# Optimization experiments

Hardware: AMD Instinct MI355X
Metric: run time of the kernel (lower is better)

The kernel has to match this reference:

```python
import jax, jax.numpy as jnp
import numpy as np

GAMMA = 3.0
R = 0.02
ALPHA_RAISE = 1.0
DW_FLOOR = 0.0
B, D, G = 2097152, 16, 2048


def _annuity_factor(tau):
    # |R| >= 1e-12, so closed form branch of _annuity_factor
    return (1.0 - jnp.exp(-R * tau)) / R


def setup_inputs() -> dict:
    key = jax.random.key(0)
    k1, k2, k3, k4, k5 = jax.random.split(key, 5)
    X = jax.random.uniform(k1, (B, 2), jnp.float32, 0.1, 2.0)      # [wealth, habit] > 0
    TmT = jax.random.uniform(k2, (B, 1), jnp.float32, 0.0, 1.0)    # time-to-maturity tau
    y = jax.random.uniform(k3, (B, 1), jnp.float32, 0.1, 1.0)      # shadow price (lambda)
    u_star = jax.random.uniform(k4, (D,), jnp.float32, 0.0, 1.0)   # Merton weights buffer
    s_grid = jnp.linspace(0.0, 1.0, G).astype(jnp.float32)         # sorted tau grid
    z_tilde = jax.random.uniform(k5, (G,), jnp.float32, 0.5, 1.5)  # RIM boundary values
    return {"X": X, "TmT": TmT, "y": y, "u_star": u_star, "s_grid": s_grid, "z_tilde": z_tilde}


def reference(X, TmT, y, u_star, s_grid, z_tilde):
    wealth = X[:, :1]
    habit = X[:, 1:2]
    tau = TmT

    # z*(t) = linear interpolation of z_tilde over s_grid (replaces CPU bisect loop)
    s = jnp.clip(tau.reshape(-1), 0.0, s_grid[-1])
    z_tau = jnp.interp(s, s_grid, z_tilde).reshape(tau.shape)

    # hit-and-raise: CRRA boundary consumption C_boundary = (z/y)^{1/gamma}
    y_eff = jnp.clip(y, 1e-12, None)
    c_on_boundary = jnp.power(jnp.clip(z_tau / y_eff, 1e-24, None), 1.0 / GAMMA)
    need_raise = (y_eff * jnp.power(habit, GAMMA)) <= z_tau
    c_raised = ALPHA_RAISE * c_on_boundary + (1.0 - ALPHA_RAISE) * habit
    C = jnp.where(need_raise, jnp.maximum(c_raised, habit), habit)
    # c_softcap is None -> no cap

    pvC = _annuity_factor(tau) * C
    dw_share = jnp.clip((wealth - pvC) / jnp.clip(wealth, 1e-12, None), DW_FLOOR, 1.0)
    u = u_star[None, :] * dw_share  # [B, D]
    return jnp.concatenate([u, C], axis=1)  # [B, D+1]
```

## Files before the change

kernel.cpp:

```cpp
#include <hip/hip_runtime.h>


#define NCOL 17
#define BLK 256
#define SLAB (BLK * NCOL)
#define SLAB4 (SLAB / 4)

typedef float f32x4 __attribute__((ext_vector_type(4)));

template<bool EXACT>
__global__ __launch_bounds__(BLK) void ratchet_kernel(
    const float* __restrict__ X,
    const float* __restrict__ TmT,
    const float* __restrict__ y,
    const float* __restrict__ u_star,
    const float* __restrict__ s_grid,
    const float* __restrict__ z_tilde,
    float* __restrict__ out,
    long long B)
{
    __shared__ float s_dw[BLK];
    __shared__ float s_C[BLK];
    __shared__ float s_u[16];

    const int tid = threadIdx.x;
    const long long row = (long long)blockIdx.x * BLK + tid;
    const long long rowc = (EXACT || row < B) ? row : (B - 1);

    if (tid < 16) s_u[tid] = u_star[tid];

    const float2 xh = ((const float2*)X)[rowc];
    const float wealth = xh.x;
    const float habit  = xh.y;
    const float tau    = TmT[rowc];
    const float yv     = y[rowc];

    float s = fminf(fmaxf(tau, 0.0f), 1.0f);
    int idx = (int)(s * 2047.0f);
    idx = idx < 2046 ? idx : 2046;
    idx = idx > 0 ? idx : 0;
    float g0 = s_grid[idx];
    float g1 = s_grid[idx + 1];
    if (s < g0 && idx > 0) {
        --idx; g1 = g0; g0 = s_grid[idx];
    } else if (s >= g1 && idx < 2046) {
        ++idx; g0 = g1; g1 = s_grid[idx + 1];
    }
    const float z0 = z_tilde[idx];
    const float z1 = z_tilde[idx + 1];
    const float frac = (s - g0) / (g1 - g0);
    const float z = z0 + (z1 - z0) * frac;

    const float y_eff = fmaxf(yv, 1e-12f);
    const float ratio = fmaxf(z / y_eff, 1e-24f);
    const float c_b   = cbrtf(ratio);
    const float h3    = habit * habit * habit;
    const float C     = (y_eff * h3 <= z) ? fmaxf(c_b, habit) : habit;
    const float ann   = (1.0f - expf(-0.02f * tau)) * 50.0f;
    const float pvC   = ann * C;
    float dw = (wealth - pvC) / fmaxf(wealth, 1e-12f);
    dw = fminf(fmaxf(dw, 0.0f), 1.0f);

    s_dw[tid] = dw;
    s_C[tid]  = C;
    __syncthreads();

    const long long slab_base = (long long)blockIdx.x * SLAB;
    f32x4* out4 = (f32x4*)(out + slab_base);

    if (EXACT) {
        #pragma unroll
        for (int it = 0; it < 4; ++it) {
            const int m = tid + it * BLK;
            const int e = 4 * m;
            float v[4];
            #pragma unroll
            for (int j = 0; j < 4; ++j) {
                const unsigned ee = (unsigned)(e + j);
                const unsigned r  = ee / 17u;
                const unsigned c  = ee - r * 17u;
                v[j] = (c < 16u) ? s_u[c] * s_dw[r] : s_C[r];
            }
            f32x4 pack = { v[0], v[1], v[2], v[3] };
            out4[m] = pack;
        }
        if (tid < SLAB4 - 4 * BLK) {
            const int m = tid + 4 * BLK;
            const int e = 4 * m;
            float v[4];
            #pragma unroll
            for (int j = 0; j < 4; ++j) {
                const unsigned ee = (unsigned)(e + j);
                const unsigned r  = ee / 17u;
                const unsigned c  = ee - r * 17u;
                v[j] = (c < 16u) ? s_u[c] * s_dw[r] : s_C[r];
            }
            f32x4 pack = { v[0], v[1], v[2], v[3] };
            out4[m] = pack;
        }
    } else {
        const long long total = B * NCOL;
        for (int m = tid; m < SLAB4; m += BLK) {
            const int e = 4 * m;
            const long long g = slab_base + e;
            float v[4];
            #pragma unroll
            for (int j = 0; j < 4; ++j) {
                const unsigned ee = (unsigned)(e + j);
                const unsigned r  = ee / 17u;
                const unsigned c  = ee - r * 17u;
                v[j] = (c < 16u) ? s_u[c] * s_dw[r] : s_C[r];
            }
            if (g + 3 < total) {
                f32x4 pack = { v[0], v[1], v[2], v[3] };
                out4[m] = pack;
            } else {
                for (int j = 0; j < 4 && g + j < total; ++j)
                    out[g + j] = v[j];
            }
        }
    }
}

extern "C" void kernel_launch(void* const* d_in, const int* in_sizes, int n_in,
                              void* d_out, int out_size, void* d_ws, size_t ws_size,
                              hipStream_t stream) {
    const float* X       = (const float*)d_in[0];
    const float* TmT     = (const float*)d_in[1];
    const float* y       = (const float*)d_in[2];
    const float* u_star  = (const float*)d_in[3];
    const float* s_grid  = (const float*)d_in[4];
    const float* z_tilde = (const float*)d_in[5];
    float* out = (float*)d_out;

    const long long B = in_sizes[1];
    const int blocks = (int)((B + BLK - 1) / BLK);
    if (B % BLK == 0) {
        ratchet_kernel<true><<<blocks, BLK, 0, stream>>>(
            X, TmT, y, u_star, s_grid, z_tilde, out, B);
    } else {
        ratchet_kernel<false><<<blocks, BLK, 0, stream>>>(
            X, TmT, y, u_star, s_grid, z_tilde, out, B);
    }
}
```

Baseline: 34.28 us.

## Use persistent grid-stride blocks with double-buffered shared memory and input prefetch

Replaces the one-block-per-slab launch with a capped persistent grid, where each block loops over several slabs. Each block prefetches the next slab's inputs into registers before storing the current slab, and alternates between two shared buffers so a single barrier per iteration is enough. This aims to overlap input loads with output stores and cut block launch overhead. It also reduces the number of waves in flight, which may lower the memory-level parallelism available to this bandwidth-bound kernel.

```diff
diff --git a/kernel.cpp b/kernel.cpp
--- a/kernel.cpp
+++ b/kernel.cpp
@@ -5,36 +5,15 @@
 #define BLK 256
 #define SLAB (BLK * NCOL)
 #define SLAB4 (SLAB / 4)
+#define PERSIST_BLOCKS 2048
 
 typedef float f32x4 __attribute__((ext_vector_type(4)));
 
-template<bool EXACT>
-__global__ __launch_bounds__(BLK) void ratchet_kernel(
-    const float* __restrict__ X,
-    const float* __restrict__ TmT,
-    const float* __restrict__ y,
-    const float* __restrict__ u_star,
-    const float* __restrict__ s_grid,
-    const float* __restrict__ z_tilde,
-    float* __restrict__ out,
-    long long B)
+__device__ __forceinline__ void compute_row(
+    float wealth, float habit, float tau, float yv,
+    const float* __restrict__ s_grid, const float* __restrict__ z_tilde,
+    float& dw_out, float& C_out)
 {
-    __shared__ float s_dw[BLK];
-    __shared__ float s_C[BLK];
-    __shared__ float s_u[16];
-
-    const int tid = threadIdx.x;
-    const long long row = (long long)blockIdx.x * BLK + tid;
-    const long long rowc = (EXACT || row < B) ? row : (B - 1);
-
-    if (tid < 16) s_u[tid] = u_star[tid];
-
-    const float2 xh = ((const float2*)X)[rowc];
-    const float wealth = xh.x;
-    const float habit  = xh.y;
-    const float tau    = TmT[rowc];
-    const float yv     = y[rowc];
-
     float s = fminf(fmaxf(tau, 0.0f), 1.0f);
     int idx = (int)(s * 2047.0f);
     idx = idx < 2046 ? idx : 2046;
@@ -60,64 +39,120 @@
     const float pvC   = ann * C;
     float dw = (wealth - pvC) / fmaxf(wealth, 1e-12f);
     dw = fminf(fmaxf(dw, 0.0f), 1.0f);
+    dw_out = dw;
+    C_out  = C;
+}
 
+__device__ __forceinline__ void store_slab(
+    f32x4* __restrict__ out4, const float* __restrict__ s_dw,
+    const float* __restrict__ s_C, const float* __restrict__ s_u, int tid)
+{
+    #pragma unroll
+    for (int it = 0; it < 5; ++it) {
+        const int m = tid + it * BLK;
+        if (it == 4 && m >= SLAB4) break;
+        const int e = 4 * m;
+        float v[4];
+        #pragma unroll
+        for (int j = 0; j < 4; ++j) {
+            const unsigned ee = (unsigned)(e + j);
+            const unsigned r  = ee / 17u;
+            const unsigned c  = ee - r * 17u;
+            v[j] = (c < 16u) ? s_u[c] * s_dw[r] : s_C[r];
+        }
+        f32x4 pack = { v[0], v[1], v[2], v[3] };
+        out4[m] = pack;
+    }
+}
+
+__global__ __launch_bounds__(BLK) void ratchet_persist(
+    const float* __restrict__ X, const float* __restrict__ TmT,
+    const float* __restrict__ y, const float* __restrict__ u_star,
+    const float* __restrict__ s_grid, const float* __restrict__ z_tilde,
+    float* __restrict__ out, long long nslabs)
+{
+    __shared__ float s_dw[2][BLK];
+    __shared__ float s_C[2][BLK];
+    __shared__ float s_u[16];
+
+    const int tid = threadIdx.x;
+    if (tid < 16) s_u[tid] = u_star[tid];
+
+    long long slab = blockIdx.x;
+    if (slab >= nslabs) return;
+
+    long long row = slab * BLK + tid;
+    float2 xh  = ((const float2*)X)[row];
+    float  tau = TmT[row];
+    float  yv  = y[row];
+
+    int buf = 0;
+    while (true) {
+        float dw, C;
+        compute_row(xh.x, xh.y, tau, yv, s_grid, z_tilde, dw, C);
+        s_dw[buf][tid] = dw;
+        s_C [buf][tid] = C;
+
+        const long long next = slab + gridDim.x;
+        if (next < nslabs) {
+            const long long nrow = next * BLK + tid;
+            xh  = ((const float2*)X)[nrow];
+            tau = TmT[nrow];
+            yv  = y[nrow];
+        }
+        __syncthreads();
+
+        store_slab((f32x4*)(out + slab * SLAB), s_dw[buf], s_C[buf], s_u, tid);
+
+        if (next >= nslabs) break;
+        slab = next;
+        buf ^= 1;
+    }
+}
+
+__global__ __launch_bounds__(BLK) void ratchet_generic(
+    const float* __restrict__ X, const float* __restrict__ TmT,
+    const float* __restrict__ y, const float* __restrict__ u_star,
+    const float* __restrict__ s_grid, const float* __restrict__ z_tilde,
+    float* __restrict__ out, long long B)
+{
+    __shared__ float s_dw[BLK];
+    __shared__ float s_C[BLK];
+    __shared__ float s_u[16];
+
+    const int tid = threadIdx.x;
+    const long long row = (long long)blockIdx.x * BLK + tid;
+    const long long rowc = row < B ? row : (B - 1);
+    if (tid < 16) s_u[tid] = u_star[tid];
+
+    const float2 xh = ((const float2*)X)[rowc];
+    float dw, C;
+    compute_row(xh.x, xh.y, TmT[rowc], y[rowc], s_grid, z_tilde, dw, C);
     s_dw[tid] = dw;
     s_C[tid]  = C;
     __syncthreads();
 
     const long long slab_base = (long long)blockIdx.x * SLAB;
     f32x4* out4 = (f32x4*)(out + slab_base);
+    const long long total = B * NCOL;
 
-    if (EXACT) {
+    for (int m = tid; m < SLAB4; m += BLK) {
+        const int e = 4 * m;
+        const long long g = slab_base + e;
+        float v[4];
         #pragma unroll
-        for (int it = 0; it < 4; ++it) {
-            const int m = tid + it * BLK;
-            const int e = 4 * m;
-            float v[4];
-            #pragma unroll
-            for (int j = 0; j < 4; ++j) {
-                const unsigned ee = (unsigned)(e + j);
-                const unsigned r  = ee / 17u;
-                const unsigned c  = ee - r * 17u;
-                v[j] = (c < 16u) ? s_u[c] * s_dw[r] : s_C[r];
-            }
+        for (int j = 0; j < 4; ++j) {
+            const unsigned ee = (unsigned)(e + j);
+            const unsigned r  = ee / 17u;
+            const unsigned c  = ee - r * 17u;
+            v[j] = (c < 16u) ? s_u[c] * s_dw[r] : s_C[r];
+        }
+        if (g + 3 < total) {
             f32x4 pack = { v[0], v[1], v[2], v[3] };
             out4[m] = pack;
-        }
-        if (tid < SLAB4 - 4 * BLK) {
-            const int m = tid + 4 * BLK;
-            const int e = 4 * m;
-            float v[4];
-            #pragma unroll
-            for (int j = 0; j < 4; ++j) {
-                const unsigned ee = (unsigned)(e + j);
-                const unsigned r  = ee / 17u;
-                const unsigned c  = ee - r * 17u;
-                v[j] = (c < 16u) ? s_u[c] * s_dw[r] : s_C[r];
-            }
-            f32x4 pack = { v[0], v[1], v[2], v[3] };
-            out4[m] = pack;
-        }
-    } else {
-        const long long total = B * NCOL;
-        for (int m = tid; m < SLAB4; m += BLK) {
-            const int e = 4 * m;
-            const long long g = slab_base + e;
-            float v[4];
-            #pragma unroll
-            for (int j = 0; j < 4; ++j) {
-                const unsigned ee = (unsigned)(e + j);
-                const unsigned r  = ee / 17u;
-                const unsigned c  = ee - r * 17u;
-                v[j] = (c < 16u) ? s_u[c] * s_dw[r] : s_C[r];
-            }
-            if (g + 3 < total) {
-                f32x4 pack = { v[0], v[1], v[2], v[3] };
-                out4[m] = pack;
-            } else {
-                for (int j = 0; j < 4 && g + j < total; ++j)
-                    out[g + j] = v[j];
-            }
+        } else {
+            for (int j = 0; j < 4 && g + j < total; ++j)
+                out[g + j] = v[j];
         }
     }
 }
@@ -134,12 +169,15 @@
     float* out = (float*)d_out;
 
     const long long B = in_sizes[1];
-    const int blocks = (int)((B + BLK - 1) / BLK);
     if (B % BLK == 0) {
-        ratchet_kernel<true><<<blocks, BLK, 0, stream>>>(
-            X, TmT, y, u_star, s_grid, z_tilde, out, B);
+        const long long nslabs = B / BLK;
+        const int blocks = (int)(nslabs < PERSIST_BLOCKS ? nslabs
+                                                         : PERSIST_BLOCKS);
+        ratchet_persist<<<blocks, BLK, 0, stream>>>(
+            X, TmT, y, u_star, s_grid, z_tilde, out, nslabs);
     } else {
-        ratchet_kernel<false><<<blocks, BLK, 0, stream>>>(
+        const int blocks = (int)((B + BLK - 1) / BLK);
+        ratchet_generic<<<blocks, BLK, 0, stream>>>(
             X, TmT, y, u_star, s_grid, z_tilde, out, B);
     }
 }
```

New measurement: 36.41 us. 1.06x slower.
